# Kernel tuning notes

Hardware: AMD Instinct MI355X
Metric: run time of the kernel (lower is better)

## Reference

```python
import jax, jax.numpy as jnp
import numpy as np

NNZ = 3355443          # int(4096*4096*(1-0.8))
IN_FEATURES = 4096
OUT_FEATURES = 4096
BATCH = 64
ACTIVE_THRESHOLD = 0.01


def setup_inputs() -> dict:
    key = jax.random.key(0)
    k1, k2, k3, k4 = jax.random.split(key, 4)
    x = jax.random.uniform(k1, (BATCH, IN_FEATURES), dtype=jnp.float32)
    row_indices = jax.random.randint(k2, (NNZ,), 0, OUT_FEATURES, dtype=jnp.int32)
    col_indices = jax.random.randint(k3, (NNZ,), 0, IN_FEATURES, dtype=jnp.int32)
    values = jax.random.normal(k4, (NNZ,), dtype=jnp.float32)
    bias = jnp.zeros((OUT_FEATURES,), dtype=jnp.float32)
    return {"x": x, "row_indices": row_indices, "col_indices": col_indices,
            "values": values, "bias": bias}


def reference(x, row_indices, col_indices, values, bias):
    # Event-driven gating: only columns with x > threshold contribute.
    # Equivalent to masking x, then a standard COO spmv per batch row.
    xm = jnp.where(x > ACTIVE_THRESHOLD, x, jnp.zeros((), x.dtype))   # [B, in]
    contrib = values[None, :] * xm[:, col_indices]                    # [B, nnz]
    out = jnp.zeros((x.shape[0], bias.shape[0]), dtype=x.dtype)
    out = out.at[:, row_indices].add(contrib)                         # scatter-add over rows
    return out + bias[None, :]
```

## Files before the change

### kernel.cpp

```cpp
#include <hip/hip_runtime.h>
#include <hip/hip_bf16.h>
#include <stdint.h>

#define IN_F 4096
#define OUT_F 4096
#define NBKT 512
#define SBLOCKS 410
#define REC_PER_SB 8192
#define SMAX 7168u
#define THRESH 0.01f

typedef unsigned int u32;
typedef unsigned short u16;
typedef __attribute__((ext_vector_type(8))) short short8;
typedef __attribute__((ext_vector_type(4))) float f32x4;

static constexpr size_t pad256(size_t x) { return (x + 255u) & ~(size_t)255u; }
static constexpr size_t WS_XB   = 0;
static constexpr size_t WS_CUR  = pad256(WS_XB + (size_t)512 * 64 * 8 * 2);
static constexpr size_t WS_BINS = pad256(WS_CUR + (size_t)NBKT * 4);
static constexpr size_t WS_NEEDED = WS_BINS + (size_t)NBKT * SMAX * 4;

static __device__ __forceinline__ u16 f2bf(float v) {
  __hip_bfloat16 h = __float2bfloat16(v);
  return *reinterpret_cast<u16*>(&h);
}

__global__ __launch_bounds__(512) void k_init(u32* __restrict__ gcursor) {
  gcursor[threadIdx.x] = 0u;
}

__global__ __launch_bounds__(1024) void k_scatter(const int* __restrict__ rows,
                                                  const int* __restrict__ cols,
                                                  const float* __restrict__ vals, u32 nnz,
                                                  const float* __restrict__ x,
                                                  u16* __restrict__ xB,
                                                  u32* __restrict__ gcursor,
                                                  u32* __restrict__ sortb) {
  __shared__ u32 cnt[NBKT];
  __shared__ u32 pref[NBKT + 1];
  __shared__ u32 gbase[NBKT];
  __shared__ u32 srt[REC_PER_SB];
  __shared__ u16 srtb[REC_PER_SB];
  const int tid = threadIdx.x;
  const int lane = tid & 63;
  const int wid = tid >> 6;

  if (blockIdx.x < 32) {
    const int g = blockIdx.x * 1024 + tid;
    const int b = g & 63;
    const int kg = g >> 6;
    const float* src = x + (size_t)b * IN_F + kg * 8;
    const f32x4 a0 = *reinterpret_cast<const f32x4*>(src);
    const f32x4 a1 = *reinterpret_cast<const f32x4*>(src + 4);
    short8 o;
#pragma unroll
    for (int e = 0; e < 4; ++e) {
      float v = a0[e]; v = (v > THRESH) ? v : 0.0f; o[e] = (short)f2bf(v);
    }
#pragma unroll
    for (int e = 0; e < 4; ++e) {
      float v = a1[e]; v = (v > THRESH) ? v : 0.0f; o[4 + e] = (short)f2bf(v);
    }
    *reinterpret_cast<short8*>(xB + ((size_t)kg * 64 + b) * 8) = o;
  }

  if (tid < NBKT) cnt[tid] = 0;
  __syncthreads();
  const u32 base_i = blockIdx.x * (u32)REC_PER_SB;
  u32 rec[8], bkt[8], rk[8];
#pragma unroll
  for (int j = 0; j < 8; ++j) {
    const u32 i = base_i + (u32)j * 1024u + tid;
    bkt[j] = 0xffffffffu;
    if (i < nnz) {
      const u32 r = (u32)rows[i] & 4095u;
      const u32 c = (u32)cols[i] & 4095u;
      rec[j] = (c << 20) | ((r & 7u) << 16) | (u32)f2bf(vals[i]);
      bkt[j] = r >> 3;
      rk[j] = atomicAdd(&cnt[bkt[j]], 1u);
    }
  }
  __syncthreads();
  if (wid == 0) {
    u32 a[8]; u32 s = 0;
#pragma unroll
    for (int j = 0; j < 8; ++j) { a[j] = cnt[lane * 8 + j]; s += a[j]; }
    u32 xx = s;
#pragma unroll
    for (int d = 1; d < 64; d <<= 1) {
      const u32 y = (u32)__shfl_up((int)xx, d, 64);
      if (lane >= d) xx += y;
    }
    u32 e = xx - s;
#pragma unroll
    for (int j = 0; j < 8; ++j) { pref[lane * 8 + j] = e; e += a[j]; }
    if (lane == 63) pref[NBKT] = e;
  }
  __syncthreads();
#pragma unroll
  for (int j = 0; j < 8; ++j)
    if (bkt[j] != 0xffffffffu) {
      const u32 pos = pref[bkt[j]] + rk[j];
      srt[pos] = rec[j];
      srtb[pos] = (u16)bkt[j];
    }
  if (tid < NBKT) {
    const u32 len = pref[tid + 1] - pref[tid];
    gbase[tid] = len ? atomicAdd(&gcursor[tid], len) : 0u;
  }
  __syncthreads();
  const u32 tot = pref[NBKT];
#pragma unroll
  for (int j = 0; j < 8; ++j) {
    const u32 i = (u32)j * 1024u + tid;
    if (i < tot) {
      const u32 t = srtb[i];
      const u32 off = gbase[t] + (i - pref[t]);
      if (off < SMAX) sortb[(size_t)t * SMAX + off] = srt[i];
    }
  }
}

__global__ __launch_bounds__(1024, 8) void k_accum(const u32* __restrict__ sortb,
                                                   const u32* __restrict__ ntot,
                                                   const u16* __restrict__ xB,
                                                   const float* __restrict__ bias,
                                                   float* __restrict__ out) {
  __shared__ float W[8 * 1024];
  const int tid = threadIdx.x;
  const int lane = tid & 63;
  const int w = tid >> 6;
  const u32 t = blockIdx.x;
  u32 n = ntot[t];
  if (n > SMAX) n = SMAX;
  const u32* bin = sortb + (size_t)t * SMAX;
  u32 rec[7];
#pragma unroll
  for (int j = 0; j < 7; ++j) {
    const u32 i = (u32)j * 1024u + tid;
    rec[j] = (i < n) ? bin[i] : 0u;
  }

  const f32x4 zv = {0.f, 0.f, 0.f, 0.f};
  f32x4 acc0 = zv, acc1 = zv, acc2 = zv, acc3 = zv;
  const int row = lane & 15;
  const bool alive = row < 8;
  const int rw = row & 7;
  const int e8 = (lane >> 4) * 8;

  for (int q = 0; q < 4; ++q) {
    __syncthreads();
#pragma unroll
    for (int j = 0; j < 2; ++j)
      *reinterpret_cast<f32x4*>(&W[j * 4096 + tid * 4]) = zv;
    __syncthreads();
#pragma unroll
    for (int j = 0; j < 7; ++j) {
      const u32 i = (u32)j * 1024u + tid;
      if (i < n) {
        const u32 rc = rec[j];
        if ((rc >> 30) == (u32)q) {
          const u32 rl = (rc >> 16) & 7u;
          const u32 cl = ((rc >> 20) & 1023u) ^ (rl << 3);
          unsafeAtomicAdd(&W[rl * 1024u + cl], __uint_as_float(rc << 16));
        }
      }
    }
    __syncthreads();
#pragma unroll
    for (int s = 0; s < 2; ++s) {
      const int klb = w * 64 + s * 32 + e8;
      const int sw = klb ^ (rw << 3);
      f32x4 wa = *reinterpret_cast<const f32x4*>(&W[rw * 1024 + sw]);
      f32x4 wb = *reinterpret_cast<const f32x4*>(&W[rw * 1024 + (sw + 4)]);
      if (!alive) { wa = zv; wb = zv; }
      short8 af;
#pragma unroll
      for (int e = 0; e < 4; ++e) af[e] = (short)f2bf(wa[e]);
#pragma unroll
      for (int e = 0; e < 4; ++e) af[4 + e] = (short)f2bf(wb[e]);
      const int kabs = q * 1024 + klb;
      const u16* bp = xB + (size_t)(kabs >> 3) * 512 + (u32)row * 8;
      const short8 b0 = *reinterpret_cast<const short8*>(bp);
      const short8 b1 = *reinterpret_cast<const short8*>(bp + 128);
      const short8 b2 = *reinterpret_cast<const short8*>(bp + 256);
      const short8 b3 = *reinterpret_cast<const short8*>(bp + 384);
      acc0 = __builtin_amdgcn_mfma_f32_16x16x32_bf16(af, b0, acc0, 0, 0, 0);
      acc1 = __builtin_amdgcn_mfma_f32_16x16x32_bf16(af, b1, acc1, 0, 0, 0);
      acc2 = __builtin_amdgcn_mfma_f32_16x16x32_bf16(af, b2, acc2, 0, 0, 0);
      acc3 = __builtin_amdgcn_mfma_f32_16x16x32_bf16(af, b3, acc3, 0, 0, 0);
    }
  }
  __syncthreads();
  {
    const int ccol = lane & 15;
    const int rb = (lane >> 4) * 4;
    if (rb < 8) {
#pragma unroll
      for (int qq = 0; qq < 4; ++qq) W[((w * 4 + 0) * 8 + rb + qq) * 16 + ccol] = acc0[qq];
#pragma unroll
      for (int qq = 0; qq < 4; ++qq) W[((w * 4 + 1) * 8 + rb + qq) * 16 + ccol] = acc1[qq];
#pragma unroll
      for (int qq = 0; qq < 4; ++qq) W[((w * 4 + 2) * 8 + rb + qq) * 16 + ccol] = acc2[qq];
#pragma unroll
      for (int qq = 0; qq < 4; ++qq) W[((w * 4 + 3) * 8 + rb + qq) * 16 + ccol] = acc3[qq];
    }
  }
  __syncthreads();
  if (tid < 512) {
    const int rl = tid & 7;
    const int b = tid >> 3;
    float sum = bias[t * 8u + rl];
#pragma unroll
    for (int w2 = 0; w2 < 16; ++w2)
      sum += W[((w2 * 4 + (b >> 4)) * 8 + rl) * 16 + (b & 15)];
    out[(size_t)b * OUT_F + t * 8u + rl] = sum;
  }
}

__global__ __launch_bounds__(256) void k_bias_init(const float* __restrict__ bias,
                                                   float* __restrict__ out) {
  const int i = blockIdx.x * 256 + threadIdx.x;
  if (i < 64 * OUT_F) out[i] = bias[i & (OUT_F - 1)];
}

__global__ __launch_bounds__(256) void k_fallback(const int* __restrict__ rows,
                                                  const int* __restrict__ cols,
                                                  const float* __restrict__ vals,
                                                  const float* __restrict__ x,
                                                  float* __restrict__ out, int nnz) {
  const int gw = (int)(((u32)blockIdx.x * blockDim.x + threadIdx.x) >> 6);
  const int lane = threadIdx.x & 63;
  const int nw = (int)(((u32)gridDim.x * blockDim.x) >> 6);
  for (int i = gw; i < nnz; i += nw) {
    const int r = rows[i];
    const int c = cols[i];
    const float v = vals[i];
    const float xv = x[lane * IN_F + c];
    if (xv > THRESH) atomicAdd(&out[(size_t)lane * OUT_F + r], v * xv);
  }
}

extern "C" void kernel_launch(void* const* d_in, const int* in_sizes, int n_in,
                              void* d_out, int out_size, void* d_ws, size_t ws_size,
                              hipStream_t stream) {
  const float* x = (const float*)d_in[0];
  const int* rows = (const int*)d_in[1];
  const int* cols = (const int*)d_in[2];
  const float* vals = (const float*)d_in[3];
  const float* bias = (const float*)d_in[4];
  float* out = (float*)d_out;
  const int nnz = in_sizes[1];

  if (ws_size >= WS_NEEDED && nnz <= SBLOCKS * REC_PER_SB) {
    u16* xB = (u16*)((char*)d_ws + WS_XB);
    u32* gcursor = (u32*)((char*)d_ws + WS_CUR);
    u32* sortb = (u32*)((char*)d_ws + WS_BINS);
    k_init<<<1, 512, 0, stream>>>(gcursor);
    k_scatter<<<SBLOCKS, 1024, 0, stream>>>(rows, cols, vals, (u32)nnz, x, xB,
                                            gcursor, sortb);
    k_accum<<<NBKT, 1024, 0, stream>>>(sortb, gcursor, xB, bias, out);
  } else {
    k_bias_init<<<(64 * OUT_F + 255) / 256, 256, 0, stream>>>(bias, out);
    k_fallback<<<4096, 256, 0, stream>>>(rows, cols, vals, x, out, nnz);
  }
}
```

Measured before the change: 62.89 us.

## Densify full 8x4096 row slab in LDS in one pass instead of four quarters

The accumulate kernel now holds the whole 8-row by 4096-column dense slab in shared memory (128 KB) instead of four 1024-column quarter passes. Each record is streamed from global memory once and scatter-added without the per-quarter filtering and extra barriers, and each wave then runs 8 MFMA steps over its 256-column slice. This removes three zero/scatter/sync rounds and the repeated record checks, but the larger LDS footprint cuts occupancy to about one 1024-thread block per CU, which the launch bound now reflects.

```diff
diff --git a/kernel.cpp b/kernel.cpp
--- a/kernel.cpp
+++ b/kernel.cpp
@@ -122,12 +122,12 @@
   }
 }
 
-__global__ __launch_bounds__(1024, 8) void k_accum(const u32* __restrict__ sortb,
+__global__ __launch_bounds__(1024, 4) void k_accum(const u32* __restrict__ sortb,
                                                    const u32* __restrict__ ntot,
                                                    const u16* __restrict__ xB,
                                                    const float* __restrict__ bias,
                                                    float* __restrict__ out) {
-  __shared__ float W[8 * 1024];
+  __shared__ float W[8 * 4096];
   const int tid = threadIdx.x;
   const int lane = tid & 63;
   const int w = tid >> 6;
@@ -135,62 +135,56 @@
   u32 n = ntot[t];
   if (n > SMAX) n = SMAX;
   const u32* bin = sortb + (size_t)t * SMAX;
-  u32 rec[7];
-#pragma unroll
-  for (int j = 0; j < 7; ++j) {
-    const u32 i = (u32)j * 1024u + tid;
-    rec[j] = (i < n) ? bin[i] : 0u;
-  }
 
   const f32x4 zv = {0.f, 0.f, 0.f, 0.f};
+#pragma unroll
+  for (int j = 0; j < 8; ++j)
+    *reinterpret_cast<f32x4*>(&W[j * 4096 + tid * 4]) = zv;
+  __syncthreads();
+
+#define ADDREC(RC) do {                                                   \
+    const u32 rl_ = ((RC) >> 16) & 7u;                                    \
+    const u32 cl_ = ((RC) >> 20) ^ (rl_ << 3);    \
+    unsafeAtomicAdd(&W[rl_ * 4096u + cl_], __uint_as_float((RC) << 16));  \
+  } while (0)
+  u32 i = (u32)tid;
+  for (; i + 3072u < n; i += 4096u) {
+    const u32 r0 = bin[i];
+    const u32 r1 = bin[i + 1024u];
+    const u32 r2 = bin[i + 2048u];
+    const u32 r3 = bin[i + 3072u];
+    ADDREC(r0); ADDREC(r1); ADDREC(r2); ADDREC(r3);
+  }
+  for (; i < n; i += 1024u) { const u32 r0 = bin[i]; ADDREC(r0); }
+#undef ADDREC
+  __syncthreads();
+
   f32x4 acc0 = zv, acc1 = zv, acc2 = zv, acc3 = zv;
   const int row = lane & 15;
   const bool alive = row < 8;
   const int rw = row & 7;
   const int e8 = (lane >> 4) * 8;
-
-  for (int q = 0; q < 4; ++q) {
-    __syncthreads();
-#pragma unroll
-    for (int j = 0; j < 2; ++j)
-      *reinterpret_cast<f32x4*>(&W[j * 4096 + tid * 4]) = zv;
-    __syncthreads();
-#pragma unroll
-    for (int j = 0; j < 7; ++j) {
-      const u32 i = (u32)j * 1024u + tid;
-      if (i < n) {
-        const u32 rc = rec[j];
-        if ((rc >> 30) == (u32)q) {
-          const u32 rl = (rc >> 16) & 7u;
-          const u32 cl = ((rc >> 20) & 1023u) ^ (rl << 3);
-          unsafeAtomicAdd(&W[rl * 1024u + cl], __uint_as_float(rc << 16));
-        }
-      }
-    }
-    __syncthreads();
-#pragma unroll
-    for (int s = 0; s < 2; ++s) {
-      const int klb = w * 64 + s * 32 + e8;
-      const int sw = klb ^ (rw << 3);
-      f32x4 wa = *reinterpret_cast<const f32x4*>(&W[rw * 1024 + sw]);
-      f32x4 wb = *reinterpret_cast<const f32x4*>(&W[rw * 1024 + (sw + 4)]);
-      if (!alive) { wa = zv; wb = zv; }
-      short8 af;
-#pragma unroll
-      for (int e = 0; e < 4; ++e) af[e] = (short)f2bf(wa[e]);
-#pragma unroll
-      for (int e = 0; e < 4; ++e) af[4 + e] = (short)f2bf(wb[e]);
-      const int kabs = q * 1024 + klb;
-      const u16* bp = xB + (size_t)(kabs >> 3) * 512 + (u32)row * 8;
-      const short8 b0 = *reinterpret_cast<const short8*>(bp);
-      const short8 b1 = *reinterpret_cast<const short8*>(bp + 128);
-      const short8 b2 = *reinterpret_cast<const short8*>(bp + 256);
-      const short8 b3 = *reinterpret_cast<const short8*>(bp + 384);
-      acc0 = __builtin_amdgcn_mfma_f32_16x16x32_bf16(af, b0, acc0, 0, 0, 0);
-      acc1 = __builtin_amdgcn_mfma_f32_16x16x32_bf16(af, b1, acc1, 0, 0, 0);
-      acc2 = __builtin_amdgcn_mfma_f32_16x16x32_bf16(af, b2, acc2, 0, 0, 0);
-      acc3 = __builtin_amdgcn_mfma_f32_16x16x32_bf16(af, b3, acc3, 0, 0, 0);
-    }
+#pragma unroll
+  for (int s = 0; s < 8; ++s) {
+    const int klb = w * 256 + s * 32 + e8;
+    const int sw = klb ^ (rw << 3);
+    f32x4 wa = *reinterpret_cast<const f32x4*>(&W[rw * 4096 + sw]);
+    f32x4 wb = *reinterpret_cast<const f32x4*>(&W[rw * 4096 + (sw + 4)]);
+    if (!alive) { wa = zv; wb = zv; }
+    short8 af;
+#pragma unroll
+    for (int e = 0; e < 4; ++e) af[e] = (short)f2bf(wa[e]);
+#pragma unroll
+    for (int e = 0; e < 4; ++e) af[4 + e] = (short)f2bf(wb[e]);
+    const u16* bp = xB + (size_t)(klb >> 3) * 512 + (u32)row * 8;
+    const short8 b0 = *reinterpret_cast<const short8*>(bp);
+    const short8 b1 = *reinterpret_cast<const short8*>(bp + 128);
+    const short8 b2 = *reinterpret_cast<const short8*>(bp + 256);
+    const short8 b3 = *reinterpret_cast<const short8*>(bp + 384);
+    acc0 = __builtin_amdgcn_mfma_f32_16x16x32_bf16(af, b0, acc0, 0, 0, 0);
+    acc1 = __builtin_amdgcn_mfma_f32_16x16x32_bf16(af, b1, acc1, 0, 0, 0);
+    acc2 = __builtin_amdgcn_mfma_f32_16x16x32_bf16(af, b2, acc2, 0, 0, 0);
+    acc3 = __builtin_amdgcn_mfma_f32_16x16x32_bf16(af, b3, acc3, 0, 0, 0);
   }
   __syncthreads();
   {
```

Result: faster. 59.76 us (-5.0%).
